# Performance work log

Hardware: AMD Instinct MI355X
Metric: run time of the kernel (lower is better)

The kernel has to match this reference:

```python
import jax, jax.numpy as jnp
import numpy as np

TOP_K = 2


def setup_inputs() -> dict:
    key = jax.random.key(0)
    k1, k2, k3, k4, k5 = jax.random.split(key, 5)
    B, S, H, F, E = 2, 2048, 1024, 4096, 8
    scale = 0.02
    return {
        "hidden_states": jax.random.normal(k1, (B, S, H), dtype=jnp.float32),
        "w_gate": jax.random.normal(k2, (H, E), dtype=jnp.float32) * scale,
        "w_gate_proj": jax.random.normal(k3, (E, H, F), dtype=jnp.float32) * scale,
        "w_up_proj": jax.random.normal(k4, (E, H, F), dtype=jnp.float32) * scale,
        "w_down_proj": jax.random.normal(k5, (E, F, H), dtype=jnp.float32) * scale,
    }


def reference(hidden_states, w_gate, w_gate_proj, w_up_proj, w_down_proj):
    B, S, H = hidden_states.shape
    E = w_gate_proj.shape[0]
    x = hidden_states.reshape(-1, H)  # [T, H]

    # Router: softmax in float32, then top-k (NOT renormalized, matching source).
    router_logits = x @ w_gate  # [T, E]
    routing_probs = jax.nn.softmax(router_logits.astype(jnp.float32), axis=-1)
    routing_weights, selected_experts = jax.lax.top_k(routing_probs, TOP_K)  # [T, k]
    routing_weights = routing_weights.astype(x.dtype)

    out = jnp.zeros_like(x)
    # Small fixed loop over experts; per-token weight is zero for unrouted
    # tokens, so the masked dense computation is mathematically identical to
    # the gather/index_add dispatch in the source.
    for e in range(E):
        w_e = jnp.sum(routing_weights * (selected_experts == e), axis=-1)  # [T]
        h = jax.nn.silu(x @ w_gate_proj[e]) * (x @ w_up_proj[e])  # [T, F]
        out = out + (h @ w_down_proj[e]) * w_e[:, None]
    return out.reshape(B, S, H)
```

## Files before the change

kernel.cpp:

```cpp
#include <hip/hip_runtime.h>
#include <hip/hip_bf16.h>

#define T_TOK 4096
#define HDIM  1024
#define FDIM  4096
#define NEXP  8
#define CAP   4096
#define MAXWL 128

typedef __attribute__((ext_vector_type(8))) short short8;
typedef __attribute__((ext_vector_type(4))) float floatx4;
typedef __attribute__((ext_vector_type(4))) float float4v;
typedef __attribute__((ext_vector_type(4))) unsigned short ushort4v;

__device__ __forceinline__ unsigned short f2bf(float f) {
    union { float f; unsigned int u; } v; v.f = f;
    unsigned int u = v.u;
    u += 0x7fffu + ((u >> 16) & 1u);
    return (unsigned short)(u >> 16);
}

__device__ __forceinline__ void gl2lds16(const void* g, void* l) {
    __builtin_amdgcn_global_load_lds(
        (const __attribute__((address_space(1))) unsigned int*)g,
        (__attribute__((address_space(3))) unsigned int*)l,
        16, 0, 0);
}

__global__ void k_convert_x(const float* __restrict__ x, unsigned short* __restrict__ xb) {
    int i = (blockIdx.x * 256 + threadIdx.x) * 4;
    float4v v = *(const float4v*)(x + i);
    ushort4v o = { f2bf(v[0]), f2bf(v[1]), f2bf(v[2]), f2bf(v[3]) };
    *(ushort4v*)(xb + i) = o;
}

__global__ void k_transpose_cast(const float* __restrict__ src, unsigned short* __restrict__ dst,
                                 int R, int C) {
    __shared__ float tile[64][65];
    size_t base = (size_t)blockIdx.z * (size_t)R * (size_t)C;
    int c0 = blockIdx.x * 64, r0 = blockIdx.y * 64;
    int lx = threadIdx.x & 15, ly = threadIdx.x >> 4;
#pragma unroll
    for (int i = 0; i < 4; ++i) {
        int rr = i * 16 + ly;
        float4v v = *(const float4v*)(src + base + (size_t)(r0 + rr) * C + c0 + lx * 4);
        tile[rr][lx * 4 + 0] = v[0]; tile[rr][lx * 4 + 1] = v[1];
        tile[rr][lx * 4 + 2] = v[2]; tile[rr][lx * 4 + 3] = v[3];
    }
    __syncthreads();
#pragma unroll
    for (int i = 0; i < 4; ++i) {
        int cc = i * 16 + ly;
        ushort4v o = { f2bf(tile[lx * 4 + 0][cc]), f2bf(tile[lx * 4 + 1][cc]),
                       f2bf(tile[lx * 4 + 2][cc]), f2bf(tile[lx * 4 + 3][cc]) };
        *(ushort4v*)(dst + base + (size_t)(c0 + cc) * R + r0 + lx * 4) = o;
    }
}

__global__ void k_router(const float* __restrict__ x, const float* __restrict__ wgate,
                         int* __restrict__ counts, int* __restrict__ ltok,
                         float* __restrict__ lwt) {
    int lane = threadIdx.x & 63;
    int tok = blockIdx.x * 4 + (threadIdx.x >> 6);
    const float* xr = x + (size_t)tok * HDIM;
    float acc[NEXP];
#pragma unroll
    for (int e = 0; e < NEXP; ++e) acc[e] = 0.f;
    for (int it = 0; it < HDIM / 256; ++it) {
        int h0 = it * 256 + lane * 4;
        float4v xv = *(const float4v*)(xr + h0);
#pragma unroll
        for (int j = 0; j < 4; ++j) {
            float4v w0 = *(const float4v*)(wgate + (size_t)(h0 + j) * NEXP);
            float4v w1 = *(const float4v*)(wgate + (size_t)(h0 + j) * NEXP + 4);
            float xs = xv[j];
            acc[0] += xs * w0[0]; acc[1] += xs * w0[1];
            acc[2] += xs * w0[2]; acc[3] += xs * w0[3];
            acc[4] += xs * w1[0]; acc[5] += xs * w1[1];
            acc[6] += xs * w1[2]; acc[7] += xs * w1[3];
        }
    }
#pragma unroll
    for (int off = 32; off >= 1; off >>= 1)
#pragma unroll
        for (int e = 0; e < NEXP; ++e)
            acc[e] += __shfl_xor(acc[e], off, 64);
    if (lane == 0) {
        float m = acc[0];
#pragma unroll
        for (int e = 1; e < NEXP; ++e) m = fmaxf(m, acc[e]);
        float p[NEXP], s = 0.f;
#pragma unroll
        for (int e = 0; e < NEXP; ++e) { p[e] = __expf(acc[e] - m); s += p[e]; }
        float inv = 1.f / s;
#pragma unroll
        for (int e = 0; e < NEXP; ++e) p[e] *= inv;
        int e0 = 0; float b0 = p[0];
#pragma unroll
        for (int e = 1; e < NEXP; ++e) if (p[e] > b0) { b0 = p[e]; e0 = e; }
        int e1 = -1; float b1 = -1.f;
#pragma unroll
        for (int e = 0; e < NEXP; ++e) if (e != e0 && p[e] > b1) { b1 = p[e]; e1 = e; }
        int p0 = atomicAdd(&counts[e0], 1);
        ltok[e0 * CAP + p0] = tok; lwt[e0 * CAP + p0] = b0;
        int p1 = atomicAdd(&counts[e1], 1);
        ltok[e1 * CAP + p1] = tok; lwt[e1 * CAP + p1] = b1;
    }
}

__global__ void k_prefix(const int* __restrict__ counts, int* __restrict__ offs,
                         int* __restrict__ wl, int* __restrict__ nwl) {
    if (threadIdx.x == 0) {
        int s = 0;
#pragma unroll
        for (int e = 0; e < NEXP; ++e) { offs[e] = s; s += counts[e]; }
        int n = 0;
        for (int e = 0; e < NEXP; ++e)
            for (int r = 0; r * 128 < counts[e] && n < MAXWL; ++r)
                wl[n++] = (e << 8) | r;
        nwl[0] = n;
    }
}

__global__ __launch_bounds__(256, 2)
void k_gemm1(const unsigned short* __restrict__ xb,
             const unsigned short* __restrict__ wgt,
             const unsigned short* __restrict__ wut,
             const int* __restrict__ counts, const int* __restrict__ offs,
             const int* __restrict__ ltok,
             const int* __restrict__ wl, const int* __restrict__ nwl,
             unsigned short* __restrict__ hbuf)
{
    if ((int)blockIdx.y >= nwl[0]) return;
    const int w = wl[blockIdx.y];
    const int e = w >> 8, rowtile = w & 255;
    const int M = counts[e];
    const int ftile = blockIdx.x;

    __shared__ __align__(16) unsigned short lA[128 * 32];
    __shared__ __align__(16) unsigned short lBg[64 * 32];
    __shared__ __align__(16) unsigned short lBu[64 * 32];
    __shared__ int stok[128];

    const int t = threadIdx.x;
    const int wave = t >> 6, lane = t & 63;

    if (t < 128) {
        int i = rowtile * 128 + t;
        stok[t] = (i < M) ? ltok[e * CAP + i] : ltok[e * CAP];
    }
    __syncthreads();

    const int r0 = t >> 2, k8 = t & 3;
    const unsigned short* pA0 = xb + (size_t)stok[r0] * HDIM + k8 * 8;
    const unsigned short* pA1 = xb + (size_t)stok[r0 + 64] * HDIM + k8 * 8;
    const size_t wbase = (size_t)e * FDIM * HDIM + (size_t)(ftile * 64) * HDIM;
    const unsigned short* pG0 = wgt + wbase + (size_t)r0 * HDIM + k8 * 8;
    const unsigned short* pU0 = wut + wbase + (size_t)r0 * HDIM + k8 * 8;

    unsigned short* dA0 = &lA[wave * 512];
    unsigned short* dA1 = &lA[2048 + wave * 512];
    unsigned short* dG0 = &lBg[wave * 512];
    unsigned short* dU0 = &lBu[wave * 512];

    const int wm = wave >> 1, wn = wave & 1;
    const int fr = lane & 15, kg = lane >> 4;

    floatx4 accg[4][2], accu[4][2];
#pragma unroll
    for (int mi = 0; mi < 4; ++mi)
#pragma unroll
        for (int ni = 0; ni < 2; ++ni) {
            floatx4 z = {0.f, 0.f, 0.f, 0.f};
            accg[mi][ni] = z; accu[mi][ni] = z;
        }

    for (int ks = 0; ks < HDIM / 32; ++ks) {
        gl2lds16(pA0, dA0); gl2lds16(pA1, dA1);
        gl2lds16(pG0, dG0); gl2lds16(pU0, dU0);
        pA0 += 32; pA1 += 32; pG0 += 32; pU0 += 32;
        __syncthreads();
        short8 a[4], bg[2], bu[2];
#pragma unroll
        for (int mi = 0; mi < 4; ++mi)
            a[mi] = *(const short8*)&lA[(wm * 64 + mi * 16 + fr) * 32 + kg * 8];
#pragma unroll
        for (int ni = 0; ni < 2; ++ni) {
            bg[ni] = *(const short8*)&lBg[(wn * 32 + ni * 16 + fr) * 32 + kg * 8];
            bu[ni] = *(const short8*)&lBu[(wn * 32 + ni * 16 + fr) * 32 + kg * 8];
        }
#pragma unroll
        for (int mi = 0; mi < 4; ++mi)
#pragma unroll
            for (int ni = 0; ni < 2; ++ni) {
                accg[mi][ni] = __builtin_amdgcn_mfma_f32_16x16x32_bf16(a[mi], bg[ni], accg[mi][ni], 0, 0, 0);
                accu[mi][ni] = __builtin_amdgcn_mfma_f32_16x16x32_bf16(a[mi], bu[ni], accu[mi][ni], 0, 0, 0);
            }
        __syncthreads();
    }

    const int hrow0 = offs[e] + rowtile * 128;
#pragma unroll
    for (int mi = 0; mi < 4; ++mi)
#pragma unroll
        for (int ni = 0; ni < 2; ++ni) {
            int c = ftile * 64 + wn * 32 + ni * 16 + fr;
#pragma unroll
            for (int r = 0; r < 4; ++r) {
                int rr = wm * 64 + mi * 16 + kg * 4 + r;
                if (rowtile * 128 + rr < M) {
                    float g = accg[mi][ni][r];
                    float val = (g / (1.f + __expf(-g))) * accu[mi][ni][r];
                    hbuf[(size_t)(hrow0 + rr) * FDIM + c] = f2bf(val);
                }
            }
        }
}

__global__ __launch_bounds__(256, 2)
void k_gemm2(const unsigned short* __restrict__ hbuf,
             const unsigned short* __restrict__ wdt,
             const int* __restrict__ counts, const int* __restrict__ offs,
             const int* __restrict__ ltok, const float* __restrict__ lwt,
             const int* __restrict__ wl, const int* __restrict__ nwl,
             float* __restrict__ out)
{
    if ((int)blockIdx.y >= nwl[0]) return;
    const int w = wl[blockIdx.y];
    const int e = w >> 8, rowtile = w & 255;
    const int M = counts[e];
    const int htile = blockIdx.x;
    const int khalf = blockIdx.z;

    __shared__ __align__(16) unsigned short lA[128 * 32];
    __shared__ __align__(16) unsigned short lB[128 * 32];
    __shared__ int stok[128];
    __shared__ float swt[128];

    const int t = threadIdx.x;
    const int wave = t >> 6, lane = t & 63;

    if (t < 128) {
        int i = rowtile * 128 + t;
        if (i < M) { stok[t] = ltok[e * CAP + i]; swt[t] = lwt[e * CAP + i]; }
        else       { stok[t] = 0; swt[t] = 0.f; }
    }

    const int row0 = offs[e] + rowtile * 128;
    const int r0 = t >> 2, k8 = t & 3;
    const int kofs = khalf * (FDIM / 2);
    const unsigned short* pA0 = hbuf + (size_t)(row0 + r0) * FDIM + kofs + k8 * 8;
    const unsigned short* pA1 = hbuf + (size_t)(row0 + 64 + r0) * FDIM + kofs + k8 * 8;
    const size_t wb = (size_t)e * HDIM * FDIM + (size_t)(htile * 128) * FDIM;
    const unsigned short* pB0 = wdt + wb + (size_t)r0 * FDIM + kofs + k8 * 8;
    const unsigned short* pB1 = wdt + wb + (size_t)(64 + r0) * FDIM + kofs + k8 * 8;

    unsigned short* dA0 = &lA[wave * 512];
    unsigned short* dA1 = &lA[2048 + wave * 512];
    unsigned short* dB0 = &lB[wave * 512];
    unsigned short* dB1 = &lB[2048 + wave * 512];

    const int wm = wave >> 1, wn = wave & 1;
    const int fr = lane & 15, kg = lane >> 4;

    floatx4 acc[4][4];
#pragma unroll
    for (int mi = 0; mi < 4; ++mi)
#pragma unroll
        for (int ni = 0; ni < 4; ++ni) {
            floatx4 z = {0.f, 0.f, 0.f, 0.f};
            acc[mi][ni] = z;
        }

    for (int ks = 0; ks < FDIM / 64; ++ks) {
        gl2lds16(pA0, dA0); gl2lds16(pA1, dA1);
        gl2lds16(pB0, dB0); gl2lds16(pB1, dB1);
        pA0 += 32; pA1 += 32; pB0 += 32; pB1 += 32;
        __syncthreads();
        short8 a[4], b[4];
#pragma unroll
        for (int mi = 0; mi < 4; ++mi)
            a[mi] = *(const short8*)&lA[(wm * 64 + mi * 16 + fr) * 32 + kg * 8];
#pragma unroll
        for (int ni = 0; ni < 4; ++ni)
            b[ni] = *(const short8*)&lB[(wn * 64 + ni * 16 + fr) * 32 + kg * 8];
#pragma unroll
        for (int mi = 0; mi < 4; ++mi)
#pragma unroll
            for (int ni = 0; ni < 4; ++ni)
                acc[mi][ni] = __builtin_amdgcn_mfma_f32_16x16x32_bf16(a[mi], b[ni], acc[mi][ni], 0, 0, 0);
        __syncthreads();
    }

#pragma unroll
    for (int mi = 0; mi < 4; ++mi)
#pragma unroll
        for (int ni = 0; ni < 4; ++ni) {
            int c = htile * 128 + wn * 64 + ni * 16 + fr;
#pragma unroll
            for (int r = 0; r < 4; ++r) {
                int rr = wm * 64 + mi * 16 + kg * 4 + r;
                if (rowtile * 128 + rr < M) {
                    float val = acc[mi][ni][r] * swt[rr];
                    atomicAdd(&out[(size_t)stok[rr] * HDIM + c], val);
                }
            }
        }
}

extern "C" void kernel_launch(void* const* d_in, const int* in_sizes, int n_in,
                              void* d_out, int out_size, void* d_ws, size_t ws_size,
                              hipStream_t stream) {
    const float* x     = (const float*)d_in[0];
    const float* wgate = (const float*)d_in[1];
    const float* wg    = (const float*)d_in[2];
    const float* wu    = (const float*)d_in[3];
    const float* wd    = (const float*)d_in[4];
    float* out = (float*)d_out;

    char* ws = (char*)d_ws;
    size_t off = 0;
    unsigned short* xb  = (unsigned short*)(ws + off); off += (size_t)T_TOK * HDIM * 2;
    unsigned short* wgt = (unsigned short*)(ws + off); off += (size_t)NEXP * FDIM * HDIM * 2;
    unsigned short* wut = (unsigned short*)(ws + off); off += (size_t)NEXP * FDIM * HDIM * 2;
    unsigned short* wdt = (unsigned short*)(ws + off); off += (size_t)NEXP * HDIM * FDIM * 2;
    unsigned short* hbuf= (unsigned short*)(ws + off); off += (size_t)(2 * T_TOK + 128) * FDIM * 2;
    int*   ltok   = (int*)(ws + off);   off += (size_t)NEXP * CAP * 4;
    float* lwt    = (float*)(ws + off); off += (size_t)NEXP * CAP * 4;
    int*   counts = (int*)(ws + off);   off += 256;
    int*   offs   = (int*)(ws + off);   off += 256;
    int*   wl     = (int*)(ws + off);   off += MAXWL * 4;
    int*   nwl    = (int*)(ws + off);   off += 256;

    hipMemsetAsync(counts, 0, 32, stream);
    hipMemsetAsync(out, 0, (size_t)T_TOK * HDIM * 4, stream);

    k_convert_x<<<T_TOK * HDIM / 1024, 256, 0, stream>>>(x, xb);
    k_transpose_cast<<<dim3(FDIM / 64, HDIM / 64, NEXP), 256, 0, stream>>>(wg, wgt, HDIM, FDIM);
    k_transpose_cast<<<dim3(FDIM / 64, HDIM / 64, NEXP), 256, 0, stream>>>(wu, wut, HDIM, FDIM);
    k_transpose_cast<<<dim3(HDIM / 64, FDIM / 64, NEXP), 256, 0, stream>>>(wd, wdt, FDIM, HDIM);
    k_router<<<T_TOK / 4, 256, 0, stream>>>(x, wgate, counts, ltok, lwt);
    k_prefix<<<1, 64, 0, stream>>>(counts, offs, wl, nwl);
    k_gemm1<<<dim3(FDIM / 64, 72), 256, 0, stream>>>(xb, wgt, wut, counts, offs, ltok, wl, nwl, hbuf);
    k_gemm2<<<dim3(HDIM / 128, 72, 2), 256, 0, stream>>>(hbuf, wdt, counts, offs, ltok, lwt, wl, nwl, out);
}
```

Before: 846.5 us.

## Replace gemm2 atomic scatter with buffered writes and a combine kernel

gemm2 now writes weighted partial outputs per sorted row and per K-half into a scratch buffer that reuses the weight workspace. A new combine kernel gathers the two expert slots per token and sums both halves, so the output memset and the float atomics are no longer needed. The x bf16 conversion moves into the router kernel, and gemm1's occupancy hint goes from 2 to 4 blocks per SM. The trade is extra buffer traffic and one extra launch against atomic contention, with some risk of register spills in gemm1.

After: 828.7 us. 1.02x faster.

```diff
diff --git a/kernel.cpp b/kernel.cpp
--- a/kernel.cpp
+++ b/kernel.cpp
@@ -7,6 +7,7 @@
 #define NEXP  8
 #define CAP   4096
 #define MAXWL 128
+#define OBR   (2 * T_TOK + 128)
 
 typedef __attribute__((ext_vector_type(8))) short short8;
 typedef __attribute__((ext_vector_type(4))) float floatx4;
@@ -25,13 +26,6 @@
         (const __attribute__((address_space(1))) unsigned int*)g,
         (__attribute__((address_space(3))) unsigned int*)l,
         16, 0, 0);
-}
-
-__global__ void k_convert_x(const float* __restrict__ x, unsigned short* __restrict__ xb) {
-    int i = (blockIdx.x * 256 + threadIdx.x) * 4;
-    float4v v = *(const float4v*)(x + i);
-    ushort4v o = { f2bf(v[0]), f2bf(v[1]), f2bf(v[2]), f2bf(v[3]) };
-    *(ushort4v*)(xb + i) = o;
 }
 
 __global__ void k_transpose_cast(const float* __restrict__ src, unsigned short* __restrict__ dst,
@@ -58,17 +52,21 @@
 }
 
 __global__ void k_router(const float* __restrict__ x, const float* __restrict__ wgate,
+                         unsigned short* __restrict__ xb,
                          int* __restrict__ counts, int* __restrict__ ltok,
-                         float* __restrict__ lwt) {
+                         float* __restrict__ lwt, int* __restrict__ tslot) {
     int lane = threadIdx.x & 63;
     int tok = blockIdx.x * 4 + (threadIdx.x >> 6);
     const float* xr = x + (size_t)tok * HDIM;
+    unsigned short* xbr = xb + (size_t)tok * HDIM;
     float acc[NEXP];
 #pragma unroll
     for (int e = 0; e < NEXP; ++e) acc[e] = 0.f;
     for (int it = 0; it < HDIM / 256; ++it) {
         int h0 = it * 256 + lane * 4;
         float4v xv = *(const float4v*)(xr + h0);
+        ushort4v xo = { f2bf(xv[0]), f2bf(xv[1]), f2bf(xv[2]), f2bf(xv[3]) };
+        *(ushort4v*)(xbr + h0) = xo;
 #pragma unroll
         for (int j = 0; j < 4; ++j) {
             float4v w0 = *(const float4v*)(wgate + (size_t)(h0 + j) * NEXP);
@@ -105,6 +103,8 @@
         ltok[e0 * CAP + p0] = tok; lwt[e0 * CAP + p0] = b0;
         int p1 = atomicAdd(&counts[e1], 1);
         ltok[e1 * CAP + p1] = tok; lwt[e1 * CAP + p1] = b1;
+        tslot[tok * 2]     = (e0 << 16) | p0;
+        tslot[tok * 2 + 1] = (e1 << 16) | p1;
     }
 }
 
@@ -122,7 +122,7 @@
     }
 }
 
-__global__ __launch_bounds__(256, 2)
+__global__ __launch_bounds__(256, 4)
 void k_gemm1(const unsigned short* __restrict__ xb,
              const unsigned short* __restrict__ wgt,
              const unsigned short* __restrict__ wut,
@@ -221,9 +221,9 @@
 void k_gemm2(const unsigned short* __restrict__ hbuf,
              const unsigned short* __restrict__ wdt,
              const int* __restrict__ counts, const int* __restrict__ offs,
-             const int* __restrict__ ltok, const float* __restrict__ lwt,
+             const float* __restrict__ lwt,
              const int* __restrict__ wl, const int* __restrict__ nwl,
-             float* __restrict__ out)
+             float* __restrict__ obuf)
 {
     if ((int)blockIdx.y >= nwl[0]) return;
     const int w = wl[blockIdx.y];
@@ -234,7 +234,6 @@
 
     __shared__ __align__(16) unsigned short lA[128 * 32];
     __shared__ __align__(16) unsigned short lB[128 * 32];
-    __shared__ int stok[128];
     __shared__ float swt[128];
 
     const int t = threadIdx.x;
@@ -242,8 +241,7 @@
 
     if (t < 128) {
         int i = rowtile * 128 + t;
-        if (i < M) { stok[t] = ltok[e * CAP + i]; swt[t] = lwt[e * CAP + i]; }
-        else       { stok[t] = 0; swt[t] = 0.f; }
+        swt[t] = (i < M) ? lwt[e * CAP + i] : 0.f;
     }
 
     const int row0 = offs[e] + rowtile * 128;
@@ -292,6 +290,7 @@
         __syncthreads();
     }
 
+    float* ob = obuf + (size_t)khalf * OBR * HDIM;
 #pragma unroll
     for (int mi = 0; mi < 4; ++mi)
 #pragma unroll
@@ -300,12 +299,26 @@
 #pragma unroll
             for (int r = 0; r < 4; ++r) {
                 int rr = wm * 64 + mi * 16 + kg * 4 + r;
-                if (rowtile * 128 + rr < M) {
-                    float val = acc[mi][ni][r] * swt[rr];
-                    atomicAdd(&out[(size_t)stok[rr] * HDIM + c], val);
-                }
+                if (rowtile * 128 + rr < M)
+                    ob[(size_t)(row0 + rr) * HDIM + c] = acc[mi][ni][r] * swt[rr];
             }
         }
+}
+
+__global__ void k_combine(const float* __restrict__ obuf, const int* __restrict__ tslot,
+                          const int* __restrict__ offs, float* __restrict__ out) {
+    int gid = blockIdx.x * 256 + threadIdx.x;
+    int tok = gid >> 8;
+    int c = (gid & 255) * 4;
+    int s0 = tslot[tok * 2], s1 = tslot[tok * 2 + 1];
+    size_t r0 = (size_t)(offs[s0 >> 16] + (s0 & 0xFFFF));
+    size_t r1 = (size_t)(offs[s1 >> 16] + (s1 & 0xFFFF));
+    float4v v00 = *(const float4v*)(obuf + r0 * HDIM + c);
+    float4v v01 = *(const float4v*)(obuf + ((size_t)OBR + r0) * HDIM + c);
+    float4v v10 = *(const float4v*)(obuf + r1 * HDIM + c);
+    float4v v11 = *(const float4v*)(obuf + ((size_t)OBR + r1) * HDIM + c);
+    float4v s = v00 + v01 + v10 + v11;
+    *(float4v*)(out + (size_t)tok * HDIM + c) = s;
 }
 
 extern "C" void kernel_launch(void* const* d_in, const int* in_sizes, int n_in,
@@ -324,23 +337,24 @@
     unsigned short* wgt = (unsigned short*)(ws + off); off += (size_t)NEXP * FDIM * HDIM * 2;
     unsigned short* wut = (unsigned short*)(ws + off); off += (size_t)NEXP * FDIM * HDIM * 2;
     unsigned short* wdt = (unsigned short*)(ws + off); off += (size_t)NEXP * HDIM * FDIM * 2;
-    unsigned short* hbuf= (unsigned short*)(ws + off); off += (size_t)(2 * T_TOK + 128) * FDIM * 2;
+    unsigned short* hbuf= (unsigned short*)(ws + off); off += (size_t)OBR * FDIM * 2;
     int*   ltok   = (int*)(ws + off);   off += (size_t)NEXP * CAP * 4;
     float* lwt    = (float*)(ws + off); off += (size_t)NEXP * CAP * 4;
+    int*   tslot  = (int*)(ws + off);   off += (size_t)T_TOK * 2 * 4;
     int*   counts = (int*)(ws + off);   off += 256;
     int*   offs   = (int*)(ws + off);   off += 256;
     int*   wl     = (int*)(ws + off);   off += MAXWL * 4;
     int*   nwl    = (int*)(ws + off);   off += 256;
+    float* obuf = (float*)wgt;
 
     hipMemsetAsync(counts, 0, 32, stream);
-    hipMemsetAsync(out, 0, (size_t)T_TOK * HDIM * 4, stream);
-
-    k_convert_x<<<T_TOK * HDIM / 1024, 256, 0, stream>>>(x, xb);
+
+    k_router<<<T_TOK / 4, 256, 0, stream>>>(x, wgate, xb, counts, ltok, lwt, tslot);
     k_transpose_cast<<<dim3(FDIM / 64, HDIM / 64, NEXP), 256, 0, stream>>>(wg, wgt, HDIM, FDIM);
     k_transpose_cast<<<dim3(FDIM / 64, HDIM / 64, NEXP), 256, 0, stream>>>(wu, wut, HDIM, FDIM);
     k_transpose_cast<<<dim3(HDIM / 64, FDIM / 64, NEXP), 256, 0, stream>>>(wd, wdt, FDIM, HDIM);
-    k_router<<<T_TOK / 4, 256, 0, stream>>>(x, wgate, counts, ltok, lwt);
     k_prefix<<<1, 64, 0, stream>>>(counts, offs, wl, nwl);
     k_gemm1<<<dim3(FDIM / 64, 72), 256, 0, stream>>>(xb, wgt, wut, counts, offs, ltok, wl, nwl, hbuf);
-    k_gemm2<<<dim3(HDIM / 128, 72, 2), 256, 0, stream>>>(hbuf, wdt, counts, offs, ltok, lwt, wl, nwl, out);
-}
+    k_gemm2<<<dim3(HDIM / 128, 72, 2), 256, 0, stream>>>(hbuf, wdt, counts, offs, lwt, wl, nwl, obuf);
+    k_combine<<<T_TOK * HDIM / 1024, 256, 0, stream>>>(obuf, tslot, offs, out);
+}
```
